# Kernel optimization log

Hardware: AMD Instinct MI355X
Metric: run time of the kernel (lower is better)

The kernel has to match this reference:

```python
import jax, jax.numpy as jnp
import numpy as np


def setup_inputs() -> dict:
    key = jax.random.key(0)
    k1, k2, k3, k4 = jax.random.split(key, 4)
    B, T, D, U = 32, 2048, 256, 256
    x = jax.random.normal(k1, (B, T, D), dtype=jnp.float32)
    Wz = jax.random.normal(k2, (D + U, U), dtype=jnp.float32) * 0.05
    Wr = jax.random.normal(k3, (D + U, U), dtype=jnp.float32) * 0.05
    Wh = jax.random.normal(k4, (D + U, U), dtype=jnp.float32) * 0.05
    return {"x": x, "Wz": Wz, "Wr": Wr, "Wh": Wh}


def reference(x, Wz, Wr, Wh):
    # GRU recurrence: z = sigmoid([x,h] Wz); r = sigmoid([x,h] Wr);
    # h_hat = tanh([x, r*h] Wh); h' = z*h + (1-z)*h_hat
    B = x.shape[0]
    U = Wz.shape[1]
    h0 = jnp.zeros((B, U), dtype=x.dtype)

    def step(h, x_t):
        x_h = jnp.concatenate([x_t, h], axis=-1)          # [B, D+U]
        z = jax.nn.sigmoid(x_h @ Wz)                       # [B, U]
        r = jax.nn.sigmoid(x_h @ Wr)                       # [B, U]
        x_rh = jnp.concatenate([x_t, r * h], axis=-1)      # [B, D+U]
        h_hat = jnp.tanh(x_rh @ Wh)                        # [B, U]
        new_h = z * h + (1.0 - z) * h_hat
        return new_h, new_h

    xs = jnp.swapaxes(x, 0, 1)                             # [T, B, D]
    _, ys = jax.lax.scan(step, h0, xs)                     # ys: [T, B, U]
    return jnp.swapaxes(ys, 0, 1)                          # [B, T, U]
```

## Files before the change

### kernel.cpp

```cpp
#include <hip/hip_runtime.h>
#include <hip/hip_fp16.h>
#include <stdint.h>

#define NB 32
#define NT 2048
#define ND 256
#define NU 256

typedef _Float16 f16x2 __attribute__((ext_vector_type(2)));

__device__ __forceinline__ float fdot2u(uint32_t a, uint32_t b, float c) {
#if __has_builtin(__builtin_amdgcn_fdot2)
  return __builtin_amdgcn_fdot2(__builtin_bit_cast(f16x2, a),
                                __builtin_bit_cast(f16x2, b), c, false);
#else
  f16x2 av = __builtin_bit_cast(f16x2, a);
  f16x2 bv = __builtin_bit_cast(f16x2, b);
  return c + (float)av.x * (float)bv.x + (float)av.y * (float)bv.y;
#endif
}

__device__ __forceinline__ uint32_t packh2(float lo, float hi) {
  f16x2 p;
  p.x = (_Float16)lo;
  p.y = (_Float16)hi;
  return __builtin_bit_cast(uint32_t, p);
}

__device__ __forceinline__ float rcp_fast(float x) { return __builtin_amdgcn_rcpf(x); }
__device__ __forceinline__ float sigmoid_fast(float x) {
  return rcp_fast(1.f + __expf(-x));
}
__device__ __forceinline__ float tanh_fast(float x) {
  return 1.f - 2.f * rcp_fast(1.f + __expf(2.f * x));
}

struct SRec {
  float hbuf[NU];
  alignas(16) uint32_t h2[NU / 2];
  alignas(16) uint32_t rh2[NU / 2];
  float psh[NU];
};
struct SGemm {
  float a[64][132];
  float b[64][68];
};

__global__ __launch_bounds__(512)
__attribute__((amdgpu_waves_per_eu(2, 2)))
void gru_combined(
    const float* __restrict__ x, const float* __restrict__ Wz,
    const float* __restrict__ Wr, const float* __restrict__ Wh,
    const uint32_t* __restrict__ Wf16, float* __restrict__ hstate,
    float* __restrict__ out, const float* __restrict__ Gsrc,
    float* __restrict__ Gdst, int t0r, int t0g, int recCnt, int chunkT) {
  __shared__ union SM {
    SRec r;
    SGemm g;
  } sm;
  const int tid = threadIdx.x;

  if ((int)blockIdx.x < recCnt) {
    const int b = blockIdx.x;
    const int u = tid & (NU - 1);
    const int role = tid >> 8;

    uint4 wfull[32], wh[16];
    const uint4* W4 = (const uint4*)Wf16;
    const int baseFull = role * (NU * 32) + u * 32;
#pragma unroll
    for (int j = 0; j < 32; j++) wfull[j] = W4[baseFull + j];
    const int baseH = 2 * (NU * 32) + u * 32 + role * 16;
#pragma unroll
    for (int j = 0; j < 16; j++) wh[j] = W4[baseH + j];

    float hu = 0.f;
    if (tid < NU) {
      hu = hstate[b * NU + tid];
      sm.r.hbuf[tid] = hu;
    }
    __syncthreads();
    if (tid < NU / 2) sm.r.h2[tid] = packh2(sm.r.hbuf[2 * tid], sm.r.hbuf[2 * tid + 1]);
    __syncthreads();

    const float* Gb = Gsrc + (size_t)b * NU + u;
    float* outp = out + ((size_t)b * NT + t0r) * NU + u;

    for (int tt = 0; tt < chunkT; ++tt) {
      float g0, g1 = 0.f;
      {
        const float* Gt = Gb + (size_t)(tt * 3) * NB * NU;
        if (role == 0) {
          g0 = Gt[0];
          g1 = Gt[2 * NB * NU];
        } else {
          g0 = Gt[NB * NU];
        }
      }
      float a0 = 0.f, a1 = 0.f, a2 = 0.f, a3 = 0.f;
#pragma unroll
      for (int jb = 0; jb < 32; jb++) {
        uint4 hv = *(const uint4*)&sm.r.h2[jb * 4];
        a0 = fdot2u(wfull[jb].x, hv.x, a0);
        a1 = fdot2u(wfull[jb].y, hv.y, a1);
        a2 = fdot2u(wfull[jb].z, hv.z, a2);
        a3 = fdot2u(wfull[jb].w, hv.w, a3);
      }
      const float ssum = ((a0 + a1) + (a2 + a3)) + g0;
      float zval = 0.f;
      if (role == 1) {
        const float rr = sigmoid_fast(ssum);
        const float hprev = sm.r.hbuf[u];
        const float rh = rr * hprev;
        const float rh1 = __shfl_down(rh, 1);
        if ((u & 1) == 0) sm.r.rh2[u >> 1] = packh2(rh, rh1);
      } else {
        zval = sigmoid_fast(ssum);
      }
      __syncthreads();
      float c0 = 0.f, c1 = 0.f, c2 = 0.f, c3 = 0.f;
#pragma unroll
      for (int jb = 0; jb < 16; jb++) {
        uint4 rv = *(const uint4*)&sm.r.rh2[(role * 16 + jb) * 4];
        c0 = fdot2u(wh[jb].x, rv.x, c0);
        c1 = fdot2u(wh[jb].y, rv.y, c1);
        c2 = fdot2u(wh[jb].z, rv.z, c2);
        c3 = fdot2u(wh[jb].w, rv.w, c3);
      }
      const float csum = (c0 + c1) + (c2 + c3);
      if (role == 1) sm.r.psh[u] = csum;
      __syncthreads();
      if (role == 0) {
        const float hh = tanh_fast(g1 + csum + sm.r.psh[u]);
        const float hn = zval * hu + (1.f - zval) * hh;
        hu = hn;
        outp[0] = hn;
        sm.r.hbuf[u] = hn;
        const float hn1 = __shfl_down(hn, 1);
        if ((u & 1) == 0) sm.r.h2[u >> 1] = packh2(hn, hn1);
      }
      outp += NU;
      __syncthreads();
    }
    if (role == 0) hstate[b * NU + u] = hu;

  } else if (Gdst != nullptr) {
    const int gg = (int)blockIdx.x - recCnt;
    const int mtile = gg / 12;
    const int ntile = gg - mtile * 12;
    const int g = ntile >> 2;
    const int u0 = (ntile & 3) * 64;
    const float* Wg = (g == 0) ? Wz : ((g == 1) ? Wr : Wh);
    const int ty = tid >> 4;
    const int tx = tid & 15;
    const int mbase = mtile * 128;
    float acc[4][4] = {{0.f}};

    for (int kk = 0; kk < 4; ++kk) {
      const int k0 = kk * 64;
      __syncthreads();
      {
        const int ml = tid & 127;
        const int kq = tid >> 7;
        const int m = mbase + ml;
        const int bb = m / chunkT;
        const int tt = m - bb * chunkT;
        const float* xp = x + ((size_t)bb * NT + t0g + tt) * ND + k0 + kq * 16;
#pragma unroll
        for (int v = 0; v < 4; ++v) {
          float4 xv = ((const float4*)xp)[v];
          sm.g.a[kq * 16 + v * 4 + 0][ml] = xv.x;
          sm.g.a[kq * 16 + v * 4 + 1][ml] = xv.y;
          sm.g.a[kq * 16 + v * 4 + 2][ml] = xv.z;
          sm.g.a[kq * 16 + v * 4 + 3][ml] = xv.w;
        }
      }
      {
        const int nl = (tid & 15) * 4;
        const int kr = tid >> 4;
#pragma unroll
        for (int s = 0; s < 2; ++s) {
          const int krow = kr + s * 32;
          float4 wv = *(const float4*)&Wg[(size_t)(k0 + krow) * NU + u0 + nl];
          *(float4*)&sm.g.b[krow][nl] = wv;
        }
      }
      __syncthreads();
#pragma unroll 8
      for (int k = 0; k < 64; ++k) {
        const float4 av = *(const float4*)&sm.g.a[k][ty * 4];
        const float4 bv = *(const float4*)&sm.g.b[k][tx * 4];
        acc[0][0] += av.x * bv.x; acc[0][1] += av.x * bv.y; acc[0][2] += av.x * bv.z; acc[0][3] += av.x * bv.w;
        acc[1][0] += av.y * bv.x; acc[1][1] += av.y * bv.y; acc[1][2] += av.y * bv.z; acc[1][3] += av.y * bv.w;
        acc[2][0] += av.z * bv.x; acc[2][1] += av.z * bv.y; acc[2][2] += av.z * bv.z; acc[2][3] += av.z * bv.w;
        acc[3][0] += av.w * bv.x; acc[3][1] += av.w * bv.y; acc[3][2] += av.w * bv.z; acc[3][3] += av.w * bv.w;
      }
    }
#pragma unroll
    for (int i = 0; i < 4; ++i) {
      const int m = mbase + ty * 4 + i;
      const int bb = m / chunkT;
      const int tt = m - bb * chunkT;
      float4 val;
      val.x = acc[i][0]; val.y = acc[i][1]; val.z = acc[i][2]; val.w = acc[i][3];
      *(float4*)&Gdst[((size_t)(tt * 3 + g) * NB + bb) * NU + u0 + tx * 4] = val;
    }
  }
}

__global__ void gru_prep(const float* __restrict__ Wz, const float* __restrict__ Wr,
                         const float* __restrict__ Wh, uint32_t* __restrict__ Wf16,
                         float* __restrict__ hstate) {
  const int idx = blockIdx.x * 256 + threadIdx.x;
  const int NW = 3 * NU * 128;
  if (idx < NW) {
    const int g = idx / (NU * 128);
    const int rem = idx - g * (NU * 128);
    const int u = rem >> 7;
    const int p = rem & 127;
    const float* Wg = (g == 0) ? Wz : ((g == 1) ? Wr : Wh);
    float w0 = Wg[(size_t)(ND + 2 * p) * NU + u];
    float w1 = Wg[(size_t)(ND + 2 * p + 1) * NU + u];
    Wf16[idx] = packh2(w0, w1);
  } else {
    const int j = idx - NW;
    if (j < NB * NU) hstate[j] = 0.f;
  }
}

extern "C" void kernel_launch(void* const* d_in, const int* in_sizes, int n_in,
                              void* d_out, int out_size, void* d_ws, size_t ws_size,
                              hipStream_t stream) {
  (void)in_sizes; (void)n_in; (void)out_size;
  const float* x = (const float*)d_in[0];
  const float* Wz = (const float*)d_in[1];
  const float* Wr = (const float*)d_in[2];
  const float* Wh = (const float*)d_in[3];
  float* out = (float*)d_out;

  int ct = 8;
  const int cands[6] = {256, 128, 64, 32, 16, 8};
  for (int i = 0; i < 6; ++i) {
    size_t need = 2ull * cands[i] * 3 * NB * NU * 4 + (1u << 20);
    if (need <= ws_size) { ct = cands[i]; break; }
  }
  const int nch = NT / ct;
  const size_t chunkBytes = (size_t)ct * 3 * NB * NU * 4;

  char* wsb = (char*)d_ws;
  float* G0 = (float*)wsb;
  float* G1 = (float*)(wsb + chunkBytes);
  uint32_t* Wf16 = (uint32_t*)(wsb + 2 * chunkBytes);
  float* hstate = (float*)(wsb + 2 * chunkBytes + (size_t)3 * NU * 128 * 4);

  const int prepThreads = 3 * NU * 128 + NB * NU;
  gru_prep<<<(prepThreads + 255) / 256, 256, 0, stream>>>(Wz, Wr, Wh, Wf16, hstate);

  gru_combined<<<3 * ct, 512, 0, stream>>>(x, Wz, Wr, Wh, Wf16, hstate, out,
                                           nullptr, G0, 0, 0, 0, ct);
  for (int k = 0; k < nch; ++k) {
    float* Gsrc = (k & 1) ? G1 : G0;
    float* Gdst = (k & 1) ? G0 : G1;
    const int gemmOn = (k + 1 < nch) ? 1 : 0;
    gru_combined<<<32 + (gemmOn ? 3 * ct : 0), 512, 0, stream>>>(
        x, Wz, Wr, Wh, Wf16, hstate, out, Gsrc, gemmOn ? Gdst : nullptr,
        k * ct, (k + 1) * ct, 32, ct);
  }
}
```

Measured before the change: 2.908 ms.

## Split recurrent dot products across 1024 threads with K-partitioned partial sums

Each recurrent block now runs 1024 threads, and each of four thread groups handles a quarter of the hidden dimension for all three gates. Partial sums are reduced through shared memory. This shortens the serial fdot2 chain per step and cuts register pressure, since each thread now holds 24 uint4 weights instead of 48. The precomputed gate inputs are prefetched one step ahead, and the GEMM tile is shrunk to 2x4 per thread to fit the larger block. The cost is an extra barrier per timestep plus more shared-memory reduction traffic.

```diff
diff --git a/kernel.cpp b/kernel.cpp
--- a/kernel.cpp
+++ b/kernel.cpp
@@ -39,16 +39,15 @@
   float hbuf[NU];
   alignas(16) uint32_t h2[NU / 2];
   alignas(16) uint32_t rh2[NU / 2];
-  float psh[NU];
+  float psA[4][2][NU];
+  float psH[4][NU];
 };
 struct SGemm {
   float a[64][132];
   float b[64][68];
 };
 
-__global__ __launch_bounds__(512)
-__attribute__((amdgpu_waves_per_eu(2, 2)))
-void gru_combined(
+__global__ __launch_bounds__(1024) void gru_combined(
     const float* __restrict__ x, const float* __restrict__ Wz,
     const float* __restrict__ Wr, const float* __restrict__ Wh,
     const uint32_t* __restrict__ Wf16, float* __restrict__ hstate,
@@ -63,86 +62,105 @@
   if ((int)blockIdx.x < recCnt) {
     const int b = blockIdx.x;
     const int u = tid & (NU - 1);
-    const int role = tid >> 8;
-
-    uint4 wfull[32], wh[16];
+    const int q = tid >> 8;
+
+    uint4 wz[8], wr[8], wh[8];
     const uint4* W4 = (const uint4*)Wf16;
-    const int baseFull = role * (NU * 32) + u * 32;
-#pragma unroll
-    for (int j = 0; j < 32; j++) wfull[j] = W4[baseFull + j];
-    const int baseH = 2 * (NU * 32) + u * 32 + role * 16;
-#pragma unroll
-    for (int j = 0; j < 16; j++) wh[j] = W4[baseH + j];
-
-    float hu = 0.f;
-    if (tid < NU) {
-      hu = hstate[b * NU + tid];
-      sm.r.hbuf[tid] = hu;
-    }
+#pragma unroll
+    for (int j = 0; j < 8; j++) wz[j] = W4[((0 * 4 + q) * 8 + j) * 256 + u];
+#pragma unroll
+    for (int j = 0; j < 8; j++) wr[j] = W4[((1 * 4 + q) * 8 + j) * 256 + u];
+#pragma unroll
+    for (int j = 0; j < 8; j++) wh[j] = W4[((2 * 4 + q) * 8 + j) * 256 + u];
+
+    const float hs = hstate[b * NU + u];
+    if (tid < NU) sm.r.hbuf[tid] = hs;
     __syncthreads();
-    if (tid < NU / 2) sm.r.h2[tid] = packh2(sm.r.hbuf[2 * tid], sm.r.hbuf[2 * tid + 1]);
+    if (tid < NU / 2)
+      sm.r.h2[tid] = packh2(sm.r.hbuf[2 * tid], sm.r.hbuf[2 * tid + 1]);
     __syncthreads();
+    float hcur = hs;
 
     const float* Gb = Gsrc + (size_t)b * NU + u;
     float* outp = out + ((size_t)b * NT + t0r) * NU + u;
 
+    float cgz = 0.f, cgr = 0.f, cgh = 0.f;
+    if (q == 0) {
+      cgz = Gb[0];
+      cgh = Gb[2 * NB * NU];
+    } else if (q == 1) {
+      cgr = Gb[NB * NU];
+    }
+
     for (int tt = 0; tt < chunkT; ++tt) {
-      float g0, g1 = 0.f;
+      float ngz = 0.f, ngr = 0.f, ngh = 0.f;
       {
-        const float* Gt = Gb + (size_t)(tt * 3) * NB * NU;
-        if (role == 0) {
-          g0 = Gt[0];
-          g1 = Gt[2 * NB * NU];
-        } else {
-          g0 = Gt[NB * NU];
+        const int tn = (tt + 1 < chunkT) ? tt + 1 : tt;
+        const float* Gt = Gb + (size_t)(tn * 3) * NB * NU;
+        if (q == 0) {
+          ngz = Gt[0];
+          ngh = Gt[2 * NB * NU];
+        } else if (q == 1) {
+          ngr = Gt[NB * NU];
         }
       }
-      float a0 = 0.f, a1 = 0.f, a2 = 0.f, a3 = 0.f;
-#pragma unroll
-      for (int jb = 0; jb < 32; jb++) {
-        uint4 hv = *(const uint4*)&sm.r.h2[jb * 4];
-        a0 = fdot2u(wfull[jb].x, hv.x, a0);
-        a1 = fdot2u(wfull[jb].y, hv.y, a1);
-        a2 = fdot2u(wfull[jb].z, hv.z, a2);
-        a3 = fdot2u(wfull[jb].w, hv.w, a3);
-      }
-      const float ssum = ((a0 + a1) + (a2 + a3)) + g0;
+      float az0 = 0.f, az1 = 0.f, ar0 = 0.f, ar1 = 0.f;
+#pragma unroll
+      for (int jb = 0; jb < 8; jb++) {
+        uint4 hv = *(const uint4*)&sm.r.h2[q * 32 + jb * 4];
+        az0 = fdot2u(wz[jb].x, hv.x, az0);
+        az1 = fdot2u(wz[jb].y, hv.y, az1);
+        az0 = fdot2u(wz[jb].z, hv.z, az0);
+        az1 = fdot2u(wz[jb].w, hv.w, az1);
+        ar0 = fdot2u(wr[jb].x, hv.x, ar0);
+        ar1 = fdot2u(wr[jb].y, hv.y, ar1);
+        ar0 = fdot2u(wr[jb].z, hv.z, ar0);
+        ar1 = fdot2u(wr[jb].w, hv.w, ar1);
+      }
+      sm.r.psA[q][0][u] = az0 + az1;
+      sm.r.psA[q][1][u] = ar0 + ar1;
+      __syncthreads();
       float zval = 0.f;
-      if (role == 1) {
-        const float rr = sigmoid_fast(ssum);
-        const float hprev = sm.r.hbuf[u];
-        const float rh = rr * hprev;
+      if (q == 0) {
+        zval = sigmoid_fast(cgz + ((sm.r.psA[0][0][u] + sm.r.psA[1][0][u]) +
+                                   (sm.r.psA[2][0][u] + sm.r.psA[3][0][u])));
+      } else if (q == 1) {
+        const float rr =
+            sigmoid_fast(cgr + ((sm.r.psA[0][1][u] + sm.r.psA[1][1][u]) +
+                                (sm.r.psA[2][1][u] + sm.r.psA[3][1][u])));
+        const float rh = rr * sm.r.hbuf[u];
         const float rh1 = __shfl_down(rh, 1);
         if ((u & 1) == 0) sm.r.rh2[u >> 1] = packh2(rh, rh1);
-      } else {
-        zval = sigmoid_fast(ssum);
-      }
-      __syncthreads();
-      float c0 = 0.f, c1 = 0.f, c2 = 0.f, c3 = 0.f;
-#pragma unroll
-      for (int jb = 0; jb < 16; jb++) {
-        uint4 rv = *(const uint4*)&sm.r.rh2[(role * 16 + jb) * 4];
-        c0 = fdot2u(wh[jb].x, rv.x, c0);
-        c1 = fdot2u(wh[jb].y, rv.y, c1);
-        c2 = fdot2u(wh[jb].z, rv.z, c2);
-        c3 = fdot2u(wh[jb].w, rv.w, c3);
-      }
-      const float csum = (c0 + c1) + (c2 + c3);
-      if (role == 1) sm.r.psh[u] = csum;
-      __syncthreads();
-      if (role == 0) {
-        const float hh = tanh_fast(g1 + csum + sm.r.psh[u]);
-        const float hn = zval * hu + (1.f - zval) * hh;
-        hu = hn;
+      }
+      __syncthreads();
+      float ah0 = 0.f, ah1 = 0.f;
+#pragma unroll
+      for (int jb = 0; jb < 8; jb++) {
+        uint4 rv = *(const uint4*)&sm.r.rh2[q * 32 + jb * 4];
+        ah0 = fdot2u(wh[jb].x, rv.x, ah0);
+        ah1 = fdot2u(wh[jb].y, rv.y, ah1);
+        ah0 = fdot2u(wh[jb].z, rv.z, ah0);
+        ah1 = fdot2u(wh[jb].w, rv.w, ah1);
+      }
+      sm.r.psH[q][u] = ah0 + ah1;
+      __syncthreads();
+      if (q == 0) {
+        const float hh = tanh_fast(cgh + ((sm.r.psH[0][u] + sm.r.psH[1][u]) +
+                                          (sm.r.psH[2][u] + sm.r.psH[3][u])));
+        const float hn = zval * hcur + (1.f - zval) * hh;
+        hcur = hn;
         outp[0] = hn;
         sm.r.hbuf[u] = hn;
         const float hn1 = __shfl_down(hn, 1);
         if ((u & 1) == 0) sm.r.h2[u >> 1] = packh2(hn, hn1);
       }
       outp += NU;
-      __syncthreads();
-    }
-    if (role == 0) hstate[b * NU + u] = hu;
+      cgz = ngz;
+      cgr = ngr;
+      cgh = ngh;
+      __syncthreads();
+    }
+    if (q == 0) hstate[b * NU + u] = hcur;
 
   } else if (Gdst != nullptr) {
     const int gg = (int)blockIdx.x - recCnt;
@@ -151,10 +169,10 @@
     const int g = ntile >> 2;
     const int u0 = (ntile & 3) * 64;
     const float* Wg = (g == 0) ? Wz : ((g == 1) ? Wr : Wh);
+    const int tx = tid & 15;
     const int ty = tid >> 4;
-    const int tx = tid & 15;
     const int mbase = mtile * 128;
-    float acc[4][4] = {{0.f}};
+    float acc[2][4] = {{0.f}};
 
     for (int kk = 0; kk < 4; ++kk) {
       const int k0 = kk * 64;
@@ -164,46 +182,42 @@
         const int kq = tid >> 7;
         const int m = mbase + ml;
         const int bb = m / chunkT;
-        const int tt = m - bb * chunkT;
-        const float* xp = x + ((size_t)bb * NT + t0g + tt) * ND + k0 + kq * 16;
-#pragma unroll
-        for (int v = 0; v < 4; ++v) {
-          float4 xv = ((const float4*)xp)[v];
-          sm.g.a[kq * 16 + v * 4 + 0][ml] = xv.x;
-          sm.g.a[kq * 16 + v * 4 + 1][ml] = xv.y;
-          sm.g.a[kq * 16 + v * 4 + 2][ml] = xv.z;
-          sm.g.a[kq * 16 + v * 4 + 3][ml] = xv.w;
-        }
+        const int ttm = m - bb * chunkT;
+        const float* xp = x + ((size_t)bb * NT + t0g + ttm) * ND + k0 + kq * 8;
+        const float4 x0 = ((const float4*)xp)[0];
+        const float4 x1 = ((const float4*)xp)[1];
+        sm.g.a[kq * 8 + 0][ml] = x0.x;
+        sm.g.a[kq * 8 + 1][ml] = x0.y;
+        sm.g.a[kq * 8 + 2][ml] = x0.z;
+        sm.g.a[kq * 8 + 3][ml] = x0.w;
+        sm.g.a[kq * 8 + 4][ml] = x1.x;
+        sm.g.a[kq * 8 + 5][ml] = x1.y;
+        sm.g.a[kq * 8 + 6][ml] = x1.z;
+        sm.g.a[kq * 8 + 7][ml] = x1.w;
       }
       {
-        const int nl = (tid & 15) * 4;
-        const int kr = tid >> 4;
-#pragma unroll
-        for (int s = 0; s < 2; ++s) {
-          const int krow = kr + s * 32;
-          float4 wv = *(const float4*)&Wg[(size_t)(k0 + krow) * NU + u0 + nl];
-          *(float4*)&sm.g.b[krow][nl] = wv;
-        }
+        const float4 wv = *(const float4*)&Wg[(size_t)(k0 + ty) * NU + u0 + tx * 4];
+        *(float4*)&sm.g.b[ty][tx * 4] = wv;
       }
       __syncthreads();
 #pragma unroll 8
       for (int k = 0; k < 64; ++k) {
-        const float4 av = *(const float4*)&sm.g.a[k][ty * 4];
+        const float2 av = *(const float2*)&sm.g.a[k][ty * 2];
         const float4 bv = *(const float4*)&sm.g.b[k][tx * 4];
-        acc[0][0] += av.x * bv.x; acc[0][1] += av.x * bv.y; acc[0][2] += av.x * bv.z; acc[0][3] += av.x * bv.w;
-        acc[1][0] += av.y * bv.x; acc[1][1] += av.y * bv.y; acc[1][2] += av.y * bv.z; acc[1][3] += av.y * bv.w;
-        acc[2][0] += av.z * bv.x; acc[2][1] += av.z * bv.y; acc[2][2] += av.z * bv.z; acc[2][3] += av.z * bv.w;
-        acc[3][0] += av.w * bv.x; acc[3][1] += av.w * bv.y; acc[3][2] += av.w * bv.z; acc[3][3] += av.w * bv.w;
-      }
-    }
-#pragma unroll
-    for (int i = 0; i < 4; ++i) {
-      const int m = mbase + ty * 4 + i;
+        acc[0][0] += av.x * bv.x; acc[0][1] += av.x * bv.y;
+        acc[0][2] += av.x * bv.z; acc[0][3] += av.x * bv.w;
+        acc[1][0] += av.y * bv.x; acc[1][1] += av.y * bv.y;
+        acc[1][2] += av.y * bv.z; acc[1][3] += av.y * bv.w;
+      }
+    }
+#pragma unroll
+    for (int i = 0; i < 2; ++i) {
+      const int m = mbase + ty * 2 + i;
       const int bb = m / chunkT;
-      const int tt = m - bb * chunkT;
+      const int ttm = m - bb * chunkT;
       float4 val;
       val.x = acc[i][0]; val.y = acc[i][1]; val.z = acc[i][2]; val.w = acc[i][3];
-      *(float4*)&Gdst[((size_t)(tt * 3 + g) * NB + bb) * NU + u0 + tx * 4] = val;
+      *(float4*)&Gdst[((size_t)(ttm * 3 + g) * NB + bb) * NU + u0 + tx * 4] = val;
     }
   }
 }
@@ -212,19 +226,20 @@
                          const float* __restrict__ Wh, uint32_t* __restrict__ Wf16,
                          float* __restrict__ hstate) {
   const int idx = blockIdx.x * 256 + threadIdx.x;
-  const int NW = 3 * NU * 128;
+  const int NW = 3 * 4 * 8 * 256 * 4;
   if (idx < NW) {
-    const int g = idx / (NU * 128);
-    const int rem = idx - g * (NU * 128);
-    const int u = rem >> 7;
-    const int p = rem & 127;
+    const int c = idx & 3;
+    const int u = (idx >> 2) & 255;
+    const int j = (idx >> 10) & 7;
+    const int q = (idx >> 13) & 3;
+    const int g = idx >> 15;
     const float* Wg = (g == 0) ? Wz : ((g == 1) ? Wr : Wh);
-    float w0 = Wg[(size_t)(ND + 2 * p) * NU + u];
-    float w1 = Wg[(size_t)(ND + 2 * p + 1) * NU + u];
+    const int k = 64 * q + 8 * j + 2 * c;
+    const float w0 = Wg[(size_t)(ND + k) * NU + u];
+    const float w1 = Wg[(size_t)(ND + k + 1) * NU + u];
     Wf16[idx] = packh2(w0, w1);
-  } else {
-    const int j = idx - NW;
-    if (j < NB * NU) hstate[j] = 0.f;
+  } else if (idx - NW < NB * NU) {
+    hstate[idx - NW] = 0.f;
   }
 }
 
@@ -253,16 +268,16 @@
   uint32_t* Wf16 = (uint32_t*)(wsb + 2 * chunkBytes);
   float* hstate = (float*)(wsb + 2 * chunkBytes + (size_t)3 * NU * 128 * 4);
 
-  const int prepThreads = 3 * NU * 128 + NB * NU;
+  const int prepThreads = 3 * 4 * 8 * 256 * 4 + NB * NU;
   gru_prep<<<(prepThreads + 255) / 256, 256, 0, stream>>>(Wz, Wr, Wh, Wf16, hstate);
 
-  gru_combined<<<3 * ct, 512, 0, stream>>>(x, Wz, Wr, Wh, Wf16, hstate, out,
-                                           nullptr, G0, 0, 0, 0, ct);
+  gru_combined<<<3 * ct, 1024, 0, stream>>>(x, Wz, Wr, Wh, Wf16, hstate, out,
+                                            nullptr, G0, 0, 0, 0, ct);
   for (int k = 0; k < nch; ++k) {
     float* Gsrc = (k & 1) ? G1 : G0;
     float* Gdst = (k & 1) ? G0 : G1;
     const int gemmOn = (k + 1 < nch) ? 1 : 0;
-    gru_combined<<<32 + (gemmOn ? 3 * ct : 0), 512, 0, stream>>>(
+    gru_combined<<<32 + (gemmOn ? 3 * ct : 0), 1024, 0, stream>>>(
         x, Wz, Wr, Wh, Wf16, hstate, out, Gsrc, gemmOn ? Gdst : nullptr,
         k * ct, (k + 1) * ct, 32, ct);
   }
```

Result: slower. 4.799 ms (+65.1%).

## Split each batch row's recurrence across 8 blocks with global-memory tick exchange

Applied to the files above, without the earlier changes.

Replaces the one-block-per-batch recurrence with 256 blocks, where each batch row is split over 8 blocks that each own 32 hidden units. The blocks exchange packed fp16 r*h and h slices every step through global memory, using tick-tagged 64-bit atomics and spin-waits. The input projection GEMM becomes a separate kernel run over large segments, storing gates as fp16 to halve workspace size, so there are far fewer launches than the per-chunk pipelined design. This trades a serial per-step block barrier chain for two cross-block spin syncs per step. It relies on all 256 blocks being co-resident to avoid deadlock, and fp16 gate storage adds rounding error.

```diff
diff --git a/kernel.cpp b/kernel.cpp
--- a/kernel.cpp
+++ b/kernel.cpp
@@ -7,6 +7,7 @@
 #define ND 256
 #define NU 256
 
+typedef unsigned long long u64;
 typedef _Float16 f16x2 __attribute__((ext_vector_type(2)));
 
 __device__ __forceinline__ float fdot2u(uint32_t a, uint32_t b, float c) {
@@ -35,197 +36,254 @@
   return 1.f - 2.f * rcp_fast(1.f + __expf(2.f * x));
 }
 
-struct SRec {
-  float hbuf[NU];
-  alignas(16) uint32_t h2[NU / 2];
-  alignas(16) uint32_t rh2[NU / 2];
-  float psh[NU];
-};
+__global__ void gru_prep(const float* __restrict__ Wz, const float* __restrict__ Wr,
+                         const float* __restrict__ Wh, uint32_t* __restrict__ Wp,
+                         uint32_t* __restrict__ exch_u32) {
+  const int idx = blockIdx.x * 256 + threadIdx.x;
+  const int NWP = 3 * 8 * 8 * 32 * 16;
+  if (idx < NWP) {
+    const int p = idx & 15;
+    const int u_l = (idx >> 4) & 31;
+    const int kq = (idx >> 9) & 7;
+    const int t3 = idx >> 12;
+    const int g = t3 % 3, s = t3 / 3;
+    const float* Wg = (g == 0) ? Wz : ((g == 1) ? Wr : Wh);
+    const int k = kq * 32 + 2 * p;
+    const int u = s * 32 + u_l;
+    Wp[idx] = packh2(Wg[(size_t)(ND + k) * NU + u], Wg[(size_t)(ND + k + 1) * NU + u]);
+  } else if (idx - NWP < 16384) {
+    exch_u32[idx - NWP] = 0u;
+  }
+}
+
 struct SGemm {
   float a[64][132];
   float b[64][68];
 };
 
-__global__ __launch_bounds__(512)
-__attribute__((amdgpu_waves_per_eu(2, 2)))
-void gru_combined(
+__global__ __launch_bounds__(512) void gru_gemm(
     const float* __restrict__ x, const float* __restrict__ Wz,
     const float* __restrict__ Wr, const float* __restrict__ Wh,
-    const uint32_t* __restrict__ Wf16, float* __restrict__ hstate,
-    float* __restrict__ out, const float* __restrict__ Gsrc,
-    float* __restrict__ Gdst, int t0r, int t0g, int recCnt, int chunkT) {
-  __shared__ union SM {
-    SRec r;
-    SGemm g;
-  } sm;
+    __half* __restrict__ Gh, int t0, int nt) {
+  __shared__ SGemm sm;
   const int tid = threadIdx.x;
-
-  if ((int)blockIdx.x < recCnt) {
-    const int b = blockIdx.x;
-    const int u = tid & (NU - 1);
-    const int role = tid >> 8;
-
-    uint4 wfull[32], wh[16];
-    const uint4* W4 = (const uint4*)Wf16;
-    const int baseFull = role * (NU * 32) + u * 32;
-#pragma unroll
-    for (int j = 0; j < 32; j++) wfull[j] = W4[baseFull + j];
-    const int baseH = 2 * (NU * 32) + u * 32 + role * 16;
-#pragma unroll
-    for (int j = 0; j < 16; j++) wh[j] = W4[baseH + j];
-
-    float hu = 0.f;
-    if (tid < NU) {
-      hu = hstate[b * NU + tid];
-      sm.r.hbuf[tid] = hu;
-    }
-    __syncthreads();
-    if (tid < NU / 2) sm.r.h2[tid] = packh2(sm.r.hbuf[2 * tid], sm.r.hbuf[2 * tid + 1]);
-    __syncthreads();
-
-    const float* Gb = Gsrc + (size_t)b * NU + u;
-    float* outp = out + ((size_t)b * NT + t0r) * NU + u;
-
-    for (int tt = 0; tt < chunkT; ++tt) {
-      float g0, g1 = 0.f;
-      {
-        const float* Gt = Gb + (size_t)(tt * 3) * NB * NU;
-        if (role == 0) {
-          g0 = Gt[0];
-          g1 = Gt[2 * NB * NU];
-        } else {
-          g0 = Gt[NB * NU];
-        }
-      }
-      float a0 = 0.f, a1 = 0.f, a2 = 0.f, a3 = 0.f;
-#pragma unroll
-      for (int jb = 0; jb < 32; jb++) {
-        uint4 hv = *(const uint4*)&sm.r.h2[jb * 4];
-        a0 = fdot2u(wfull[jb].x, hv.x, a0);
-        a1 = fdot2u(wfull[jb].y, hv.y, a1);
-        a2 = fdot2u(wfull[jb].z, hv.z, a2);
-        a3 = fdot2u(wfull[jb].w, hv.w, a3);
-      }
-      const float ssum = ((a0 + a1) + (a2 + a3)) + g0;
-      float zval = 0.f;
-      if (role == 1) {
-        const float rr = sigmoid_fast(ssum);
-        const float hprev = sm.r.hbuf[u];
-        const float rh = rr * hprev;
-        const float rh1 = __shfl_down(rh, 1);
-        if ((u & 1) == 0) sm.r.rh2[u >> 1] = packh2(rh, rh1);
-      } else {
-        zval = sigmoid_fast(ssum);
-      }
-      __syncthreads();
-      float c0 = 0.f, c1 = 0.f, c2 = 0.f, c3 = 0.f;
-#pragma unroll
-      for (int jb = 0; jb < 16; jb++) {
-        uint4 rv = *(const uint4*)&sm.r.rh2[(role * 16 + jb) * 4];
-        c0 = fdot2u(wh[jb].x, rv.x, c0);
-        c1 = fdot2u(wh[jb].y, rv.y, c1);
-        c2 = fdot2u(wh[jb].z, rv.z, c2);
-        c3 = fdot2u(wh[jb].w, rv.w, c3);
-      }
-      const float csum = (c0 + c1) + (c2 + c3);
-      if (role == 1) sm.r.psh[u] = csum;
-      __syncthreads();
-      if (role == 0) {
-        const float hh = tanh_fast(g1 + csum + sm.r.psh[u]);
-        const float hn = zval * hu + (1.f - zval) * hh;
-        hu = hn;
-        outp[0] = hn;
-        sm.r.hbuf[u] = hn;
-        const float hn1 = __shfl_down(hn, 1);
-        if ((u & 1) == 0) sm.r.h2[u >> 1] = packh2(hn, hn1);
-      }
-      outp += NU;
-      __syncthreads();
-    }
-    if (role == 0) hstate[b * NU + u] = hu;
-
-  } else if (Gdst != nullptr) {
-    const int gg = (int)blockIdx.x - recCnt;
-    const int mtile = gg / 12;
-    const int ntile = gg - mtile * 12;
-    const int g = ntile >> 2;
-    const int u0 = (ntile & 3) * 64;
-    const float* Wg = (g == 0) ? Wz : ((g == 1) ? Wr : Wh);
-    const int ty = tid >> 4;
-    const int tx = tid & 15;
-    const int mbase = mtile * 128;
-    float acc[4][4] = {{0.f}};
-
-    for (int kk = 0; kk < 4; ++kk) {
-      const int k0 = kk * 64;
-      __syncthreads();
-      {
-        const int ml = tid & 127;
-        const int kq = tid >> 7;
-        const int m = mbase + ml;
-        const int bb = m / chunkT;
-        const int tt = m - bb * chunkT;
-        const float* xp = x + ((size_t)bb * NT + t0g + tt) * ND + k0 + kq * 16;
-#pragma unroll
-        for (int v = 0; v < 4; ++v) {
-          float4 xv = ((const float4*)xp)[v];
-          sm.g.a[kq * 16 + v * 4 + 0][ml] = xv.x;
-          sm.g.a[kq * 16 + v * 4 + 1][ml] = xv.y;
-          sm.g.a[kq * 16 + v * 4 + 2][ml] = xv.z;
-          sm.g.a[kq * 16 + v * 4 + 3][ml] = xv.w;
-        }
-      }
-      {
-        const int nl = (tid & 15) * 4;
-        const int kr = tid >> 4;
-#pragma unroll
-        for (int s = 0; s < 2; ++s) {
-          const int krow = kr + s * 32;
-          float4 wv = *(const float4*)&Wg[(size_t)(k0 + krow) * NU + u0 + nl];
-          *(float4*)&sm.g.b[krow][nl] = wv;
-        }
-      }
-      __syncthreads();
+  const int gg = (int)blockIdx.x;
+  const int mtile = gg / 12;
+  const int ntile = gg - mtile * 12;
+  const int g = ntile >> 2;
+  const int u0 = (ntile & 3) * 64;
+  const float* Wg = (g == 0) ? Wz : ((g == 1) ? Wr : Wh);
+  const int ty = tid >> 4;
+  const int tx = tid & 15;
+  const int mbase = mtile * 128;
+  float acc[4][4] = {{0.f}};
+
+  for (int kk = 0; kk < 4; ++kk) {
+    const int k0 = kk * 64;
+    __syncthreads();
+    {
+      const int ml = tid & 127;
+      const int kq = tid >> 7;
+      const int m = mbase + ml;
+      const int bb = m / nt;
+      const int ttm = m - bb * nt;
+      const float* xp = x + ((size_t)bb * NT + t0 + ttm) * ND + k0 + kq * 16;
+#pragma unroll
+      for (int v = 0; v < 4; ++v) {
+        float4 xv = ((const float4*)xp)[v];
+        sm.a[kq * 16 + v * 4 + 0][ml] = xv.x;
+        sm.a[kq * 16 + v * 4 + 1][ml] = xv.y;
+        sm.a[kq * 16 + v * 4 + 2][ml] = xv.z;
+        sm.a[kq * 16 + v * 4 + 3][ml] = xv.w;
+      }
+    }
+    {
+      const int nl = (tid & 15) * 4;
+      const int kr = tid >> 4;
+#pragma unroll
+      for (int s2 = 0; s2 < 2; ++s2) {
+        const int krow = kr + s2 * 32;
+        float4 wv = *(const float4*)&Wg[(size_t)(k0 + krow) * NU + u0 + nl];
+        *(float4*)&sm.b[krow][nl] = wv;
+      }
+    }
+    __syncthreads();
 #pragma unroll 8
-      for (int k = 0; k < 64; ++k) {
-        const float4 av = *(const float4*)&sm.g.a[k][ty * 4];
-        const float4 bv = *(const float4*)&sm.g.b[k][tx * 4];
-        acc[0][0] += av.x * bv.x; acc[0][1] += av.x * bv.y; acc[0][2] += av.x * bv.z; acc[0][3] += av.x * bv.w;
-        acc[1][0] += av.y * bv.x; acc[1][1] += av.y * bv.y; acc[1][2] += av.y * bv.z; acc[1][3] += av.y * bv.w;
-        acc[2][0] += av.z * bv.x; acc[2][1] += av.z * bv.y; acc[2][2] += av.z * bv.z; acc[2][3] += av.z * bv.w;
-        acc[3][0] += av.w * bv.x; acc[3][1] += av.w * bv.y; acc[3][2] += av.w * bv.z; acc[3][3] += av.w * bv.w;
-      }
-    }
-#pragma unroll
-    for (int i = 0; i < 4; ++i) {
-      const int m = mbase + ty * 4 + i;
-      const int bb = m / chunkT;
-      const int tt = m - bb * chunkT;
-      float4 val;
-      val.x = acc[i][0]; val.y = acc[i][1]; val.z = acc[i][2]; val.w = acc[i][3];
-      *(float4*)&Gdst[((size_t)(tt * 3 + g) * NB + bb) * NU + u0 + tx * 4] = val;
-    }
-  }
-}
-
-__global__ void gru_prep(const float* __restrict__ Wz, const float* __restrict__ Wr,
-                         const float* __restrict__ Wh, uint32_t* __restrict__ Wf16,
-                         float* __restrict__ hstate) {
-  const int idx = blockIdx.x * 256 + threadIdx.x;
-  const int NW = 3 * NU * 128;
-  if (idx < NW) {
-    const int g = idx / (NU * 128);
-    const int rem = idx - g * (NU * 128);
-    const int u = rem >> 7;
-    const int p = rem & 127;
-    const float* Wg = (g == 0) ? Wz : ((g == 1) ? Wr : Wh);
-    float w0 = Wg[(size_t)(ND + 2 * p) * NU + u];
-    float w1 = Wg[(size_t)(ND + 2 * p + 1) * NU + u];
-    Wf16[idx] = packh2(w0, w1);
+    for (int k = 0; k < 64; ++k) {
+      const float4 av = *(const float4*)&sm.a[k][ty * 4];
+      const float4 bv = *(const float4*)&sm.b[k][tx * 4];
+      acc[0][0] += av.x * bv.x; acc[0][1] += av.x * bv.y; acc[0][2] += av.x * bv.z; acc[0][3] += av.x * bv.w;
+      acc[1][0] += av.y * bv.x; acc[1][1] += av.y * bv.y; acc[1][2] += av.y * bv.z; acc[1][3] += av.y * bv.w;
+      acc[2][0] += av.z * bv.x; acc[2][1] += av.z * bv.y; acc[2][2] += av.z * bv.z; acc[2][3] += av.z * bv.w;
+      acc[3][0] += av.w * bv.x; acc[3][1] += av.w * bv.y; acc[3][2] += av.w * bv.z; acc[3][3] += av.w * bv.w;
+    }
+  }
+#pragma unroll
+  for (int i = 0; i < 4; ++i) {
+    const int m = mbase + ty * 4 + i;
+    const int bb = m / nt;
+    const int ttm = m - bb * nt;
+    uint2 o;
+    o.x = packh2(acc[i][0], acc[i][1]);
+    o.y = packh2(acc[i][2], acc[i][3]);
+    *(uint2*)&Gh[((size_t)(ttm * 3 + g) * NB + bb) * NU + u0 + tx * 4] = o;
+  }
+}
+
+__global__ __launch_bounds__(256)
+__attribute__((amdgpu_waves_per_eu(1, 4)))
+void gru_rec(const uint32_t* __restrict__ Wp, const __half* __restrict__ Gh,
+             float* __restrict__ out, u64* exch, float* __restrict__ hstate,
+             int t0, int nt, int init) {
+  const int bid = (int)blockIdx.x;
+  const int bb = (bid & 7) + 8 * (bid >> 6);
+  const int s = (bid >> 3) & 7;
+  const int tid = threadIdx.x;
+  const int u_l = tid & 31;
+  const int kq = tid >> 5;
+  const int u = s * 32 + u_l;
+
+  uint4 wz[4], wr[4], wh[4];
+  {
+    const uint4* W4 = (const uint4*)Wp;
+    const int b0 = (s * 3 + 0) * 1024 + kq * 128 + u_l * 4;
+    const int b1 = (s * 3 + 1) * 1024 + kq * 128 + u_l * 4;
+    const int b2 = (s * 3 + 2) * 1024 + kq * 128 + u_l * 4;
+#pragma unroll
+    for (int j = 0; j < 4; j++) {
+      wz[j] = W4[b0 + j];
+      wr[j] = W4[b1 + j];
+      wh[j] = W4[b2 + j];
+    }
+  }
+
+  __shared__ uint32_t h2full[128], rh2full[128];
+  __shared__ float psZ[8][32], psR[8][32], psH[8][32];
+  __shared__ float zbuf[32], hown[32];
+
+  u64* exA = exch + ((size_t)bb * 8 + s) * 16;
+  u64* exB = exch + 4096 + ((size_t)bb * 8 + s) * 16;
+
+  if (init) {
+    if (tid < 128) h2full[tid] = 0u;
+    if (tid < 32) hown[tid] = 0.f;
   } else {
-    const int j = idx - NW;
-    if (j < NB * NU) hstate[j] = 0.f;
-  }
+    if (tid < 128)
+      h2full[tid] = packh2(hstate[bb * NU + 2 * tid], hstate[bb * NU + 2 * tid + 1]);
+    if (tid < 32) hown[tid] = hstate[bb * NU + s * 32 + tid];
+  }
+  __syncthreads();
+
+  float cgz = 0.f, cgr = 0.f, cgh = 0.f, ngz = 0.f, ngr = 0.f, ngh = 0.f;
+  if (tid < 32) {
+    cgz = (float)Gh[((size_t)0 * NB + bb) * NU + u];
+    cgr = (float)Gh[((size_t)1 * NB + bb) * NU + u];
+    cgh = (float)Gh[((size_t)2 * NB + bb) * NU + u];
+  }
+
+  for (int tt = 0; tt < nt; ++tt) {
+    const int gt = t0 + tt;
+    const uint32_t tickA = 2u * (uint32_t)gt + 1u;
+    const uint32_t tickB = tickA + 1u;
+
+    float a0 = 0.f, a1 = 0.f, r0 = 0.f, r1 = 0.f;
+#pragma unroll
+    for (int j = 0; j < 4; j++) {
+      const uint4 hv = *(const uint4*)&h2full[kq * 16 + j * 4];
+      a0 = fdot2u(wz[j].x, hv.x, a0);
+      a1 = fdot2u(wz[j].y, hv.y, a1);
+      a0 = fdot2u(wz[j].z, hv.z, a0);
+      a1 = fdot2u(wz[j].w, hv.w, a1);
+      r0 = fdot2u(wr[j].x, hv.x, r0);
+      r1 = fdot2u(wr[j].y, hv.y, r1);
+      r0 = fdot2u(wr[j].z, hv.z, r0);
+      r1 = fdot2u(wr[j].w, hv.w, r1);
+    }
+    psZ[kq][u_l] = a0 + a1;
+    psR[kq][u_l] = r0 + r1;
+    __syncthreads();
+    if (tid < 32) {
+      float sz = cgz, sr = cgr;
+#pragma unroll
+      for (int k = 0; k < 8; k++) {
+        sz += psZ[k][tid];
+        sr += psR[k][tid];
+      }
+      const float z = sigmoid_fast(sz);
+      const float r = sigmoid_fast(sr);
+      zbuf[tid] = z;
+      const float rh = r * hown[tid];
+      const float rhn = __shfl_down(rh, 1);
+      if ((tid & 1) == 0) {
+        const uint32_t pk = packh2(rh, rhn);
+        rh2full[s * 16 + (tid >> 1)] = pk;
+        __hip_atomic_store(&exA[tid >> 1], ((u64)tickA << 32) | pk,
+                           __ATOMIC_RELAXED, __HIP_MEMORY_SCOPE_AGENT);
+      }
+      const int tl = (tt + 1 < nt) ? tt + 1 : tt;
+      ngz = (float)Gh[((size_t)(tl * 3 + 0) * NB + bb) * NU + u];
+      ngr = (float)Gh[((size_t)(tl * 3 + 1) * NB + bb) * NU + u];
+      ngh = (float)Gh[((size_t)(tl * 3 + 2) * NB + bb) * NU + u];
+    }
+    __syncthreads();
+    if (tid < 128) {
+      const int which = tid >> 4, w = tid & 15;
+      if (which != s) {
+        const u64* p = exch + ((size_t)bb * 8 + which) * 16 + w;
+        u64 v;
+        do {
+          v = __hip_atomic_load(p, __ATOMIC_RELAXED, __HIP_MEMORY_SCOPE_AGENT);
+        } while ((uint32_t)(v >> 32) < tickA);
+        rh2full[which * 16 + w] = (uint32_t)v;
+      }
+    }
+    __syncthreads();
+    float h0 = 0.f, h1 = 0.f;
+#pragma unroll
+    for (int j = 0; j < 4; j++) {
+      const uint4 rv = *(const uint4*)&rh2full[kq * 16 + j * 4];
+      h0 = fdot2u(wh[j].x, rv.x, h0);
+      h1 = fdot2u(wh[j].y, rv.y, h1);
+      h0 = fdot2u(wh[j].z, rv.z, h0);
+      h1 = fdot2u(wh[j].w, rv.w, h1);
+    }
+    psH[kq][u_l] = h0 + h1;
+    __syncthreads();
+    if (tid < 32) {
+      float sh = cgh;
+#pragma unroll
+      for (int k = 0; k < 8; k++) sh += psH[k][tid];
+      const float hh = tanh_fast(sh);
+      const float z = zbuf[tid];
+      const float hn = z * hown[tid] + (1.f - z) * hh;
+      out[((size_t)bb * NT + gt) * NU + u] = hn;
+      hown[tid] = hn;
+      const float hnn = __shfl_down(hn, 1);
+      if ((tid & 1) == 0) {
+        const uint32_t pk = packh2(hn, hnn);
+        h2full[s * 16 + (tid >> 1)] = pk;
+        __hip_atomic_store(&exB[tid >> 1], ((u64)tickB << 32) | pk,
+                           __ATOMIC_RELAXED, __HIP_MEMORY_SCOPE_AGENT);
+      }
+      cgz = ngz;
+      cgr = ngr;
+      cgh = ngh;
+    }
+    __syncthreads();
+    if (tid < 128) {
+      const int which = tid >> 4, w = tid & 15;
+      if (which != s) {
+        const u64* p = exch + 4096 + ((size_t)bb * 8 + which) * 16 + w;
+        u64 v;
+        do {
+          v = __hip_atomic_load(p, __ATOMIC_RELAXED, __HIP_MEMORY_SCOPE_AGENT);
+        } while ((uint32_t)(v >> 32) < tickB);
+        h2full[which * 16 + w] = (uint32_t)v;
+      }
+    }
+    __syncthreads();
+  }
+  if (tid < 32) hstate[bb * NU + s * 32 + tid] = hown[tid];
 }
 
 extern "C" void kernel_launch(void* const* d_in, const int* in_sizes, int n_in,
@@ -238,32 +296,25 @@
   const float* Wh = (const float*)d_in[3];
   float* out = (float*)d_out;
 
-  int ct = 8;
-  const int cands[6] = {256, 128, 64, 32, 16, 8};
-  for (int i = 0; i < 6; ++i) {
-    size_t need = 2ull * cands[i] * 3 * NB * NU * 4 + (1u << 20);
-    if (need <= ws_size) { ct = cands[i]; break; }
-  }
-  const int nch = NT / ct;
-  const size_t chunkBytes = (size_t)ct * 3 * NB * NU * 4;
+  const size_t fixedBytes = 393216 + 65536 + 32768 + 4096;
+  size_t usable = (ws_size > fixedBytes) ? ws_size - fixedBytes : 0;
+  int segT = (int)(usable / 49152);
+  segT = (segT / 128) * 128;
+  if (segT > NT) segT = NT;
+  if (segT < 128) segT = 128;
 
   char* wsb = (char*)d_ws;
-  float* G0 = (float*)wsb;
-  float* G1 = (float*)(wsb + chunkBytes);
-  uint32_t* Wf16 = (uint32_t*)(wsb + 2 * chunkBytes);
-  float* hstate = (float*)(wsb + 2 * chunkBytes + (size_t)3 * NU * 128 * 4);
-
-  const int prepThreads = 3 * NU * 128 + NB * NU;
-  gru_prep<<<(prepThreads + 255) / 256, 256, 0, stream>>>(Wz, Wr, Wh, Wf16, hstate);
-
-  gru_combined<<<3 * ct, 512, 0, stream>>>(x, Wz, Wr, Wh, Wf16, hstate, out,
-                                           nullptr, G0, 0, 0, 0, ct);
-  for (int k = 0; k < nch; ++k) {
-    float* Gsrc = (k & 1) ? G1 : G0;
-    float* Gdst = (k & 1) ? G0 : G1;
-    const int gemmOn = (k + 1 < nch) ? 1 : 0;
-    gru_combined<<<32 + (gemmOn ? 3 * ct : 0), 512, 0, stream>>>(
-        x, Wz, Wr, Wh, Wf16, hstate, out, Gsrc, gemmOn ? Gdst : nullptr,
-        k * ct, (k + 1) * ct, 32, ct);
-  }
-}
+  __half* Gh = (__half*)wsb;
+  uint32_t* Wp = (uint32_t*)(wsb + (size_t)segT * 49152);
+  u64* exch = (u64*)(wsb + (size_t)segT * 49152 + 393216);
+  float* hstate = (float*)(wsb + (size_t)segT * 49152 + 393216 + 65536);
+
+  gru_prep<<<448, 256, 0, stream>>>(Wz, Wr, Wh, Wp, (uint32_t*)exch);
+
+  for (int t0 = 0; t0 < NT; t0 += segT) {
+    const int ntt = (NT - t0 < segT) ? (NT - t0) : segT;
+    gru_gemm<<<(NB * ntt / 128) * 12, 512, 0, stream>>>(x, Wz, Wr, Wh, Gh, t0, ntt);
+    gru_rec<<<256, 256, 0, stream>>>(Wp, Gh, out, exch, hstate, t0, ntt,
+                                     (t0 == 0) ? 1 : 0);
+  }
+}
```

Measured after the change: 4.682 ms. 1.61x slower.
